# Kernel optimization log

Measured on AMD Instinct MI355X. Metric: run time of the kernel, lower is better.

## Reference

```python
import jax, jax.numpy as jnp
import numpy as np
import math

DIM_PER_HEAD = 64

def setup_inputs() -> dict:
    key = jax.random.key(0)
    k1, k2, k3, k4 = jax.random.split(key, 4)
    B, H, S, D = 2, 16, 2048, 64
    mat1 = jax.random.normal(k1, (B, H, S, D), dtype=jnp.float32)
    mat2 = jax.random.normal(k2, (B, H, S, D), dtype=jnp.float32)
    mat3 = jax.random.normal(k3, (B, H, S, D), dtype=jnp.float32)
    bias = jax.random.normal(k4, (1, 1, S, S), dtype=jnp.float32)
    return {"mat1": mat1, "mat2": mat2, "mat3": mat3, "bias": bias}

def reference(mat1, mat2, mat3, bias) -> jnp.ndarray:
    # scale Q, scores = QK^T + bias, softmax over last dim, then @ V
    scale = 1.0 / math.sqrt(DIM_PER_HEAD)
    qk = jnp.einsum('bhqd,bhkd->bhqk', mat1 * scale, mat2)  # [B,H,S,S]
    scores = jax.nn.softmax(qk + bias, axis=-1)
    return jnp.einsum('bhqk,bhkd->bhqd', scores, mat3)
```

## Files before the change

kernel.cpp:

```cpp
#include <hip/hip_runtime.h>
#include <hip/hip_bf16.h>


#define SEQ 2048
#define DH  64
#define BHN 32
#define LOG2E 1.44269504088896f

typedef __attribute__((ext_vector_type(8))) short bf16x8;
typedef __attribute__((ext_vector_type(4))) float f32x4;
typedef __attribute__((ext_vector_type(8))) short short8v;

__device__ inline short f2b(float x) {
    union { float f; unsigned u; } v; v.f = x;
    unsigned r = v.u + 0x7fff + ((v.u >> 16) & 1);
    return (short)(r >> 16);
}

__device__ inline void gl_lds16(const void* g, void* l) {
    __builtin_amdgcn_global_load_lds(
        (const __attribute__((address_space(1))) void*)g,
        (__attribute__((address_space(3))) void*)l, 16, 0, 0);
}

__global__ __launch_bounds__(256)
void prep_kv(const float* __restrict__ K, const float* __restrict__ V,
             short* __restrict__ Kb, short* __restrict__ Vt) {
    __shared__ short t[64 * 72];
    const int tid = threadIdx.x;
    const int bh = blockIdx.x >> 5, st = blockIdx.x & 31, s0 = st * 64;

    {
        const float* Kp = K + ((size_t)bh * SEQ + s0) * DH;
        short* Ko = Kb + ((size_t)bh * SEQ + s0) * DH;
        #pragma unroll
        for (int i = 0; i < 2; ++i) {
            size_t o = (size_t)(tid + i * 256) * 8;
            f32x4 a = *(const f32x4*)(Kp + o);
            f32x4 b = *(const f32x4*)(Kp + o + 4);
            short8v s;
            #pragma unroll
            for (int j = 0; j < 4; ++j) { s[j] = f2b(a[j]); s[4 + j] = f2b(b[j]); }
            *(short8v*)(Ko + o) = s;
        }
    }

    const float* Vb = V + (size_t)bh * SEQ * DH + (size_t)s0 * DH;
    #pragma unroll
    for (int i = 0; i < 4; ++i) {
        int c = tid + i * 256, s = c >> 4, c4 = c & 15;
        f32x4 v = *(const f32x4*)(Vb + s * DH + c4 * 4);
        #pragma unroll
        for (int j = 0; j < 4; ++j) t[s * 72 + c4 * 4 + j] = f2b(v[j]);
    }
    __syncthreads();
    const int d = tid >> 2, part = tid & 3;
    short8v lo, hi;
    #pragma unroll
    for (int j = 0; j < 8; ++j) {
        lo[j] = t[(part * 16 + j) * 72 + d];
        hi[j] = t[(part * 16 + 8 + j) * 72 + d];
    }
    short* outp = Vt + (size_t)bh * DH * SEQ + (size_t)d * SEQ + s0 + part * 16;
    *(short8v*)outp = lo;
    *(short8v*)(outp + 8) = hi;
}

__global__ __launch_bounds__(256, 4)
void mha_main(const float* __restrict__ Q, const float* __restrict__ Bias,
              const short* __restrict__ Kb, const short* __restrict__ Vt,
              float* __restrict__ Out)
{
    __shared__ short lds_k[64 * DH];
    __shared__ short lds_v[DH * 64];
    __shared__ short lds_p[4 * 16 * 64];

    const int tid = threadIdx.x, lane = tid & 63, wave = tid >> 6;
    const int l15 = lane & 15, l4 = lane >> 4;
    const int qb = blockIdx.x & 31, bh = blockIdx.x >> 5;
    const int q0 = qb * 64;

    const float* Qb = Q + (size_t)bh * SEQ * DH;
    const short* Kh = Kb + (size_t)bh * SEQ * DH;
    const short* Vh = Vt + (size_t)bh * DH * SEQ;
    float* Ob = Out + (size_t)bh * SEQ * DH;

    bf16x8 qf[2];
    {
        const float* qp = Qb + (size_t)(q0 + wave * 16 + l15) * DH;
        #pragma unroll
        for (int ks = 0; ks < 2; ++ks) {
            short tmp[8];
            #pragma unroll
            for (int j = 0; j < 8; ++j) tmp[j] = f2b(qp[ks * 32 + l4 * 8 + j] * 0.125f);
            qf[ks] = *reinterpret_cast<bf16x8*>(tmp);
        }
    }

    f32x4 o_acc[4];
    #pragma unroll
    for (int dt = 0; dt < 4; ++dt) o_acc[dt] = f32x4{0.f, 0.f, 0.f, 0.f};
    float l_part[4] = {0.f, 0.f, 0.f, 0.f};

    const short* kg[2]; const short* vg[2]; short* kl[2]; short* vl[2];
    #pragma unroll
    for (int p = 0; p < 2; ++p) {
        int slot = p * 256 + wave * 64 + lane;
        int r_ = slot >> 3;
        int c_ = slot & 7;
        int cg = c_ ^ (r_ & 7);
        kg[p] = Kh + (size_t)r_ * DH + cg * 8;
        vg[p] = Vh + (size_t)r_ * SEQ + cg * 8;
        kl[p] = &lds_k[(size_t)(p * 256 + wave * 64) * 8];
        vl[p] = &lds_v[(size_t)(p * 256 + wave * 64) * 8];
    }
    const float* bp0 = Bias + (size_t)(q0 + wave * 16 + l4 * 4) * SEQ + l15;
    short* pw = &lds_p[wave * 16 * 64];
    const int swz = l15 & 7;

    for (int kt = 0; kt < SEQ / 64; ++kt) {
        const int k0 = kt * 64;
        __syncthreads();
        gl_lds16(kg[0] + (size_t)k0 * DH, kl[0]);
        gl_lds16(kg[1] + (size_t)k0 * DH, kl[1]);
        gl_lds16(vg[0] + k0, vl[0]);
        gl_lds16(vg[1] + k0, vl[1]);

        f32x4 sacc[4];
        const float* bp = bp0 + k0;
        #pragma unroll
        for (int nt = 0; nt < 4; ++nt)
            #pragma unroll
            for (int r = 0; r < 4; ++r)
                sacc[nt][r] = bp[(size_t)r * SEQ + nt * 16];

        __syncthreads();

        #pragma unroll
        for (int ks = 0; ks < 2; ++ks)
            #pragma unroll
            for (int nt = 0; nt < 4; ++nt) {
                int cc = (ks * 4 + l4) ^ swz;
                bf16x8 kf = *(const bf16x8*)&lds_k[(nt * 16 + l15) * DH + cc * 8];
                sacc[nt] = __builtin_amdgcn_mfma_f32_16x16x32_bf16(qf[ks], kf, sacc[nt], 0, 0, 0);
            }

        #pragma unroll
        for (int r = 0; r < 4; ++r) {
            const int prow = l4 * 4 + r;
            const int rsw = prow & 7;
            #pragma unroll
            for (int nt = 0; nt < 4; ++nt) {
                float pv = __builtin_amdgcn_exp2f(sacc[nt][r] * LOG2E);
                l_part[r] += pv;
                int pc = (nt * 2 + (l15 >> 3)) ^ rsw;
                pw[prow * 64 + pc * 8 + (l15 & 7)] = f2b(pv);
            }
        }

        #pragma unroll
        for (int ks = 0; ks < 2; ++ks) {
            int cc = (ks * 4 + l4) ^ swz;
            bf16x8 pf = *(const bf16x8*)&pw[l15 * 64 + cc * 8];
            #pragma unroll
            for (int dt = 0; dt < 4; ++dt) {
                bf16x8 vf = *(const bf16x8*)&lds_v[(dt * 16 + l15) * DH + cc * 8];
                o_acc[dt] = __builtin_amdgcn_mfma_f32_16x16x32_bf16(pf, vf, o_acc[dt], 0, 0, 0);
            }
        }
    }

    #pragma unroll
    for (int r = 0; r < 4; ++r) {
        float s = l_part[r];
        #pragma unroll
        for (int m = 1; m < 16; m <<= 1) s += __shfl_xor(s, m, 64);
        l_part[r] = s;
    }

    #pragma unroll
    for (int r = 0; r < 4; ++r) {
        float inv = 1.0f / l_part[r];
        float* op = Ob + (size_t)(q0 + wave * 16 + l4 * 4 + r) * DH + l15;
        #pragma unroll
        for (int dt = 0; dt < 4; ++dt) op[dt * 16] = o_acc[dt][r] * inv;
    }
}

extern "C" void kernel_launch(void* const* d_in, const int* in_sizes, int n_in,
                              void* d_out, int out_size, void* d_ws, size_t ws_size,
                              hipStream_t stream) {
    const float* Q    = (const float*)d_in[0];
    const float* K    = (const float*)d_in[1];
    const float* V    = (const float*)d_in[2];
    const float* Bias = (const float*)d_in[3];
    float* O          = (float*)d_out;

    short* Kb = (short*)d_ws;
    short* Vt = Kb + (size_t)BHN * SEQ * DH;

    prep_kv<<<dim3(BHN * 32), dim3(256), 0, stream>>>(K, V, Kb, Vt);
    mha_main<<<dim3(BHN * 32), dim3(256), 0, stream>>>(Q, Bias, Kb, Vt, O);
}
```

Measured before the change: 167.3 us.

## Double-buffer K/V tiles in LDS with prefetch and manual waitcnt barriers

Splits the K and V LDS tiles into two ping-pong buffers and issues the async global-to-LDS loads for the next tile before computing the current one, so load latency overlaps the MFMA and softmax work. Bias values are loaded into registers and added after QK^T instead of seeding the accumulator. The two __syncthreads per tile become a hand-written s_waitcnt vmcnt(20) plus s_barrier, and a second barrier at the end of each tile. This doubles K/V LDS use, which may reduce occupancy. The hard-coded vmcnt count depends on the compiler's exact load ordering, so if the count is off a wave could read a buffer before its data has arrived.

```diff
diff --git a/kernel.cpp b/kernel.cpp
--- a/kernel.cpp
+++ b/kernel.cpp
@@ -71,8 +71,10 @@
               const short* __restrict__ Kb, const short* __restrict__ Vt,
               float* __restrict__ Out)
 {
-    __shared__ short lds_k[64 * DH];
-    __shared__ short lds_v[DH * 64];
+    __shared__ short ka[64 * DH];
+    __shared__ short kbuf[64 * DH];
+    __shared__ short va[64 * DH];
+    __shared__ short vbuf[64 * DH];
     __shared__ short lds_p[4 * 16 * 64];
 
     const int tid = threadIdx.x, lane = tid & 63, wave = tid >> 6;
@@ -102,46 +104,54 @@
     for (int dt = 0; dt < 4; ++dt) o_acc[dt] = f32x4{0.f, 0.f, 0.f, 0.f};
     float l_part[4] = {0.f, 0.f, 0.f, 0.f};
 
-    const short* kg[2]; const short* vg[2]; short* kl[2]; short* vl[2];
-    #pragma unroll
-    for (int p = 0; p < 2; ++p) {
-        int slot = p * 256 + wave * 64 + lane;
-        int r_ = slot >> 3;
-        int c_ = slot & 7;
-        int cg = c_ ^ (r_ & 7);
-        kg[p] = Kh + (size_t)r_ * DH + cg * 8;
-        vg[p] = Vh + (size_t)r_ * SEQ + cg * 8;
-        kl[p] = &lds_k[(size_t)(p * 256 + wave * 64) * 8];
-        vl[p] = &lds_v[(size_t)(p * 256 + wave * 64) * 8];
+    const short *kg0, *kg1, *vg0, *vg1;
+    int off0, off1;
+    {
+        int s0_ = wave * 64 + lane, r0 = s0_ >> 3, c0 = s0_ & 7, g0 = c0 ^ (r0 & 7);
+        int s1_ = 256 + wave * 64 + lane, r1 = s1_ >> 3, c1 = s1_ & 7, g1 = c1 ^ (r1 & 7);
+        kg0 = Kh + (size_t)r0 * DH + g0 * 8;
+        vg0 = Vh + (size_t)r0 * SEQ + g0 * 8;
+        kg1 = Kh + (size_t)r1 * DH + g1 * 8;
+        vg1 = Vh + (size_t)r1 * SEQ + g1 * 8;
+        off0 = (wave * 64) * 8;
+        off1 = (256 + wave * 64) * 8;
     }
     const float* bp0 = Bias + (size_t)(q0 + wave * 16 + l4 * 4) * SEQ + l15;
     short* pw = &lds_p[wave * 16 * 64];
     const int swz = l15 & 7;
 
-    for (int kt = 0; kt < SEQ / 64; ++kt) {
-        const int k0 = kt * 64;
-        __syncthreads();
-        gl_lds16(kg[0] + (size_t)k0 * DH, kl[0]);
-        gl_lds16(kg[1] + (size_t)k0 * DH, kl[1]);
-        gl_lds16(vg[0] + k0, vl[0]);
-        gl_lds16(vg[1] + k0, vl[1]);
+    gl_lds16(kg0, ka + off0);
+    gl_lds16(kg1, ka + off1);
+    gl_lds16(vg0, va + off0);
+    gl_lds16(vg1, va + off1);
+
+    auto tile = [&](int kt, const short* kc, const short* vc,
+                    short* knx, short* vnx) {
+        const float* bp = bp0 + kt * 64;
+        float bv[4][4];
+        #pragma unroll
+        for (int r = 0; r < 4; ++r)
+            #pragma unroll
+            for (int nt = 0; nt < 4; ++nt)
+                bv[r][nt] = bp[(size_t)r * SEQ + nt * 16];
+
+        const int kn = (kt + 1) & 31;
+        gl_lds16(kg0 + (size_t)kn * 64 * DH, knx + off0);
+        gl_lds16(kg1 + (size_t)kn * 64 * DH, knx + off1);
+        gl_lds16(vg0 + kn * 64, vnx + off0);
+        gl_lds16(vg1 + kn * 64, vnx + off1);
+
+        asm volatile("s_waitcnt vmcnt(20)\n\ts_barrier" ::: "memory");
 
         f32x4 sacc[4];
-        const float* bp = bp0 + k0;
-        #pragma unroll
-        for (int nt = 0; nt < 4; ++nt)
-            #pragma unroll
-            for (int r = 0; r < 4; ++r)
-                sacc[nt][r] = bp[(size_t)r * SEQ + nt * 16];
-
-        __syncthreads();
-
+        #pragma unroll
+        for (int nt = 0; nt < 4; ++nt) sacc[nt] = f32x4{0.f, 0.f, 0.f, 0.f};
         #pragma unroll
         for (int ks = 0; ks < 2; ++ks)
             #pragma unroll
             for (int nt = 0; nt < 4; ++nt) {
                 int cc = (ks * 4 + l4) ^ swz;
-                bf16x8 kf = *(const bf16x8*)&lds_k[(nt * 16 + l15) * DH + cc * 8];
+                bf16x8 kf = *(const bf16x8*)&kc[(nt * 16 + l15) * DH + cc * 8];
                 sacc[nt] = __builtin_amdgcn_mfma_f32_16x16x32_bf16(qf[ks], kf, sacc[nt], 0, 0, 0);
             }
 
@@ -151,7 +161,7 @@
             const int rsw = prow & 7;
             #pragma unroll
             for (int nt = 0; nt < 4; ++nt) {
-                float pv = __builtin_amdgcn_exp2f(sacc[nt][r] * LOG2E);
+                float pv = __builtin_amdgcn_exp2f((sacc[nt][r] + bv[r][nt]) * LOG2E);
                 l_part[r] += pv;
                 int pc = (nt * 2 + (l15 >> 3)) ^ rsw;
                 pw[prow * 64 + pc * 8 + (l15 & 7)] = f2b(pv);
@@ -164,10 +174,17 @@
             bf16x8 pf = *(const bf16x8*)&pw[l15 * 64 + cc * 8];
             #pragma unroll
             for (int dt = 0; dt < 4; ++dt) {
-                bf16x8 vf = *(const bf16x8*)&lds_v[(dt * 16 + l15) * DH + cc * 8];
+                bf16x8 vf = *(const bf16x8*)&vc[(dt * 16 + l15) * DH + cc * 8];
                 o_acc[dt] = __builtin_amdgcn_mfma_f32_16x16x32_bf16(pf, vf, o_acc[dt], 0, 0, 0);
             }
         }
+
+        asm volatile("s_barrier" ::: "memory");
+    };
+
+    for (int kt = 0; kt < SEQ / 64; kt += 2) {
+        tile(kt,     ka,   va,   kbuf, vbuf);
+        tile(kt + 1, kbuf, vbuf, ka,   va);
     }
 
     #pragma unroll
```

New measurement: 169.5 us. No clear change (+1.3%).
